# Optimization experiments

Hardware: AMD Instinct MI355X
Metric: run time of the kernel (lower is better)

The kernel has to match this reference:

```python
import jax, jax.numpy as jnp
import numpy as np

N_NODES = 50000


def _sage_conv(x, src, dst, W_l, b_l, W_r):
    # mean aggregation of source-node features at destination nodes
    msg_sum = jax.ops.segment_sum(x[src], dst, num_segments=N_NODES)  # [N, d_in]
    deg = jax.ops.segment_sum(jnp.ones((src.shape[0],), x.dtype), dst,
                              num_segments=N_NODES)  # [N]
    mean = msg_sum / jnp.maximum(deg, 1.0)[:, None]
    # SAGEConv: lin_l(aggr) + lin_r(x); lin_l has bias, lin_r does not
    return mean @ W_l + b_l + x @ W_r


def setup_inputs() -> dict:
    key = jax.random.key(0)
    ks = jax.random.split(key, 8)
    d_in, d_hid, d_out = 128, 128, 64
    E = 800000
    s = lambda k, shp: jax.random.normal(k, shp, dtype=jnp.float32) * (1.0 / np.sqrt(shp[0]))
    return {
        "x": jax.random.normal(ks[0], (N_NODES, d_in), dtype=jnp.float32),
        "edge_index": jax.random.randint(ks[1], (2, E), 0, N_NODES, dtype=jnp.int64
                                         if jax.config.jax_enable_x64 else jnp.int32),
        "W_l1": s(ks[2], (d_in, d_hid)),
        "b_l1": jnp.zeros((d_hid,), jnp.float32),
        "W_r1": s(ks[3], (d_in, d_hid)),
        "W_l2": s(ks[4], (d_hid, d_out)),
        "b_l2": jnp.zeros((d_out,), jnp.float32),
        "W_r2": s(ks[5], (d_hid, d_out)),
    }


def reference(x, edge_index, W_l1, b_l1, W_r1, W_l2, b_l2, W_r2):
    src, dst = edge_index[0], edge_index[1]
    h = _sage_conv(x, src, dst, W_l1, b_l1, W_r1)
    h = jax.nn.relu(h)  # dropout is identity in eval mode
    h = _sage_conv(h, src, dst, W_l2, b_l2, W_r2)
    return h
```

## Files before the change

### kernel.cpp

```cpp
#include <hip/hip_runtime.h>
#include <hip/hip_bf16.h>

#define N_NODES 50000
#define M_TILES 3125
#define NBUCKET 196
#define CAP 5120
#define CHUNK_A 3125
#define CONV_BLOCKS 6250
#define QSCALE 20.0f
#define QINV   0.05f
#define PSCALE 16.0f
#define PINV   0.0625f

typedef __attribute__((ext_vector_type(8))) __bf16 bf16x8;
typedef __attribute__((ext_vector_type(4))) float f32x4;

#define OFF_OFF   0
#define OFFE_OFF  200192
#define EBUF_OFF  400384
#define GCUR_OFF  2407424
#define INV_OFF   3800576
#define XBF_OFF   4000768
#define AGG_OFF   16800768
#define PAIRS_OFF 29600768
#define PBF_OFF   42400768
#define WP1_OFF   48800768
#define WP2_OFF   48866304

__device__ __forceinline__ unsigned bfbits(float f) {
    unsigned u = __float_as_uint(f);
    return (u + 0x7fffu + ((u >> 16) & 1u)) & 0xffff0000u;
}
__device__ __forceinline__ unsigned short bf16r(float f) {
    return (unsigned short)(bfbits(f) >> 16);
}
__device__ __forceinline__ float blo(unsigned u) { return __uint_as_float(u << 16); }
__device__ __forceinline__ float bhi(unsigned u) { return __uint_as_float(u & 0xffff0000u); }

__device__ __forceinline__ unsigned f2i8s(float f, float scale) {
    int q = __float2int_rn(fminf(fmaxf(f * scale, -127.0f), 127.0f));
    return (unsigned)(q & 0xff);
}
__device__ __forceinline__ int sb(unsigned v, int by) {
    return (int)(signed char)((v >> (8 * by)) & 0xffu);
}

__global__ __launch_bounds__(256) void prepA_kernel(const float4* __restrict__ x4,
                                                    uint2* __restrict__ xbf,
                                                    unsigned* __restrict__ xq8,
                                                    const float* __restrict__ Wl1,
                                                    const float* __restrict__ Wr1,
                                                    const float* __restrict__ Wl2,
                                                    const float* __restrict__ Wr2,
                                                    unsigned short* __restrict__ Wp1,
                                                    unsigned short* __restrict__ Wp2,
                                                    const int* __restrict__ src,
                                                    const int* __restrict__ dst,
                                                    int* __restrict__ gcur,
                                                    unsigned* __restrict__ pairs, int E) {
    __shared__ int bh[256];
    __shared__ int lcur[256];
    __shared__ int gb[256];
    __shared__ int sc[256];
    __shared__ unsigned lbuf[3328];
    int bid = blockIdx.x;
    int t = threadIdx.x;
    if (bid < CONV_BLOCKS) {
        int i = bid * 256 + t;
        float4 v = x4[i];
        uint2 o;
        o.x = (bfbits(v.x) >> 16) | bfbits(v.y);
        o.y = (bfbits(v.z) >> 16) | bfbits(v.w);
        xbf[i] = o;
        xq8[i] = f2i8s(v.x, QSCALE) | (f2i8s(v.y, QSCALE) << 8) |
                 (f2i8s(v.z, QSCALE) << 16) | (f2i8s(v.w, QSCALE) << 24);
        return;
    }
    bid -= CONV_BLOCKS;
    if (bid < 128) {
        int idx = bid * 256 + t;
        int k = idx >> 7, n = idx & 127;
        float v = (k < 128) ? Wl1[k * 128 + n] : Wr1[(k - 128) * 128 + n];
        Wp1[((k >> 5) << 12) + (n << 5) + (((k >> 3) & 3) << 3) + (k & 7)] = bf16r(v);
        return;
    }
    bid -= 128;
    if (bid < 64) {
        int idx = bid * 256 + t;
        int k = idx >> 7, n = idx & 127;
        float v = (n < 64) ? Wl2[k * 64 + n] : Wr2[k * 64 + (n - 64)];
        Wp2[((k >> 5) << 12) + (n << 5) + (((k >> 3) & 3) << 3) + (k & 7)] = bf16r(v);
        return;
    }
    bid -= 64;
    int e0 = bid * CHUNK_A;
    int e1 = min(e0 + CHUNK_A, E);
    bh[t] = 0;
    lcur[t] = 0;
    __syncthreads();
    for (int e = e0 + t; e < e1; e += 256) atomicAdd(&bh[dst[e] >> 8], 1);
    __syncthreads();
    int v = bh[t];
    sc[t] = v;
    __syncthreads();
    for (int d = 1; d < 256; d <<= 1) {
        int u = (t >= d) ? sc[t - d] : 0;
        __syncthreads();
        sc[t] += u;
        __syncthreads();
    }
    int lbase = sc[t] - v;
    if (v > 0) gb[t] = t * CAP + atomicAdd(&gcur[t], v);
    bh[t] = lbase;
    __syncthreads();
    for (int e = e0 + t; e < e1; e += 256) {
        int s = src[e], d = dst[e];
        int b = d >> 8;
        int lpos = bh[b] + atomicAdd(&lcur[b], 1);
        lbuf[lpos] = (unsigned)s | ((unsigned)d << 16);
    }
    __syncthreads();
    int T = e1 - e0;
    for (int k = t; k < T; k += 256) {
        unsigned p = lbuf[k];
        int b = p >> 24;
        pairs[gb[b] + (k - bh[b])] = p;
    }
}

__global__ __launch_bounds__(256) void passB_kernel(const int* __restrict__ gcur,
                                                    const unsigned* __restrict__ pairs,
                                                    int* __restrict__ off,
                                                    int* __restrict__ offE,
                                                    float* __restrict__ invdeg,
                                                    unsigned short* __restrict__ ebuf16) {
    __shared__ int sc[256];
    __shared__ int fh[256];
    __shared__ int lcnt[256];
    __shared__ unsigned short lout[CAP];
    int b = blockIdx.x;
    int t = threadIdx.x;
    int gb = b * CAP;
    int W = gcur[b];
    fh[t] = 0;
    __syncthreads();
    for (int k = t; k < W; k += 256) atomicAdd(&fh[(pairs[gb + k] >> 16) & 255], 1);
    __syncthreads();
    int c = fh[t];
    sc[t] = c;
    __syncthreads();
    for (int d = 1; d < 256; d <<= 1) {
        int u = (t >= d) ? sc[t - d] : 0;
        __syncthreads();
        sc[t] += u;
        __syncthreads();
    }
    int excl = sc[t] - c;
    int dg = b * 256 + t;
    if (dg < N_NODES) {
        off[dg] = gb + excl;
        offE[dg] = gb + excl + c;
        invdeg[dg] = 1.0f / fmaxf((float)c, 1.0f);
    }
    lcnt[t] = excl;
    __syncthreads();
    for (int k = t; k < W; k += 256) {
        unsigned p = pairs[gb + k];
        int dl = (p >> 16) & 255;
        int pos = atomicAdd(&lcnt[dl], 1);
        lout[pos] = (unsigned short)(p & 0xffffu);
    }
    __syncthreads();
    for (int k = t; k < W; k += 256) ebuf16[gb + k] = lout[k];
}

__global__ __launch_bounds__(64) void gather1_kernel(const int* __restrict__ off,
                                                     const int* __restrict__ offE,
                                                     const unsigned short* __restrict__ ebuf,
                                                     const float* __restrict__ invdeg,
                                                     const uint2* __restrict__ xq8,
                                                     uint4* __restrict__ aggbf4) {
    int d = blockIdx.x;
    int j = threadIdx.x;
    int g = j >> 4;
    int f = j & 15;
    int lo = off[d], hi = offE[d];
    int a[8] = {0, 0, 0, 0, 0, 0, 0, 0};
    int i = lo + g;
    for (; i + 12 < hi; i += 16) {
        int s0 = ebuf[i], s1 = ebuf[i + 4], s2 = ebuf[i + 8], s3 = ebuf[i + 12];
        uint2 v0 = xq8[(size_t)s0 * 16 + f];
        uint2 v1 = xq8[(size_t)s1 * 16 + f];
        uint2 v2 = xq8[(size_t)s2 * 16 + f];
        uint2 v3 = xq8[(size_t)s3 * 16 + f];
#pragma unroll
        for (int by = 0; by < 4; ++by) {
            a[by]     += sb(v0.x, by) + sb(v1.x, by) + sb(v2.x, by) + sb(v3.x, by);
            a[4 + by] += sb(v0.y, by) + sb(v1.y, by) + sb(v2.y, by) + sb(v3.y, by);
        }
    }
    for (; i < hi; i += 4) {
        uint2 v = xq8[(size_t)ebuf[i] * 16 + f];
#pragma unroll
        for (int by = 0; by < 4; ++by) {
            a[by]     += sb(v.x, by);
            a[4 + by] += sb(v.y, by);
        }
    }
#pragma unroll
    for (int q = 0; q < 8; ++q) {
        a[q] += __shfl_xor(a[q], 16, 64);
        a[q] += __shfl_xor(a[q], 32, 64);
    }
    if (g == 0) {
        float inv = invdeg[d] * QINV;
        uint4 o;
        o.x = (bfbits(a[0] * inv) >> 16) | bfbits(a[1] * inv);
        o.y = (bfbits(a[2] * inv) >> 16) | bfbits(a[3] * inv);
        o.z = (bfbits(a[4] * inv) >> 16) | bfbits(a[5] * inv);
        o.w = (bfbits(a[6] * inv) >> 16) | bfbits(a[7] * inv);
        aggbf4[(size_t)d * 16 + f] = o;
    }
}

__global__ __launch_bounds__(256) void gemmF_kernel(const unsigned short* __restrict__ aggbf,
                                                    const unsigned short* __restrict__ xbf,
                                                    const unsigned short* __restrict__ Wp1,
                                                    const float* __restrict__ b1,
                                                    const unsigned short* __restrict__ Wp2,
                                                    const float* __restrict__ b2,
                                                    unsigned char* __restrict__ pq8,
                                                    float* __restrict__ out) {
    __shared__ unsigned short hsm[4][2][2048];
    int w = threadIdx.x >> 6;
    int pairIdx = blockIdx.x * 4 + w;
    int tile0 = pairIdx * 2;
    int tile1 = tile0 + 1;
    bool act0 = tile0 < M_TILES;
    bool act1 = tile1 < M_TILES;
    int t0 = act0 ? tile0 : 0;
    int t1 = act1 ? tile1 : 0;
    int lane = threadIdx.x & 63;
    int lo16 = lane & 15;
    int kg = lane >> 4;
    int r0 = kg * 4;

    f32x4 accA[8], accB[8];
#pragma unroll
    for (int n = 0; n < 8; ++n) {
        accA[n] = (f32x4){0.f, 0.f, 0.f, 0.f};
        accB[n] = (f32x4){0.f, 0.f, 0.f, 0.f};
    }
    const unsigned short* rowa0 = aggbf + (size_t)(t0 * 16 + lo16) * 128;
    const unsigned short* rowx0 = xbf + (size_t)(t0 * 16 + lo16) * 128;
    const unsigned short* rowa1 = aggbf + (size_t)(t1 * 16 + lo16) * 128;
    const unsigned short* rowx1 = xbf + (size_t)(t1 * 16 + lo16) * 128;
#pragma unroll
    for (int ks = 0; ks < 8; ++ks) {
        int ao = (ks < 4 ? ks * 32 : (ks - 4) * 32) + kg * 8;
        bf16x8 a0 = *reinterpret_cast<const bf16x8*>((ks < 4 ? rowa0 : rowx0) + ao);
        bf16x8 a1 = *reinterpret_cast<const bf16x8*>((ks < 4 ? rowa1 : rowx1) + ao);
        const unsigned short* wbase = Wp1 + ks * 4096 + lo16 * 32 + kg * 8;
#pragma unroll
        for (int n = 0; n < 8; ++n) {
            bf16x8 b = *reinterpret_cast<const bf16x8*>(wbase + n * 512);
            accA[n] = __builtin_amdgcn_mfma_f32_16x16x32_bf16(a0, b, accA[n], 0, 0, 0);
            accB[n] = __builtin_amdgcn_mfma_f32_16x16x32_bf16(a1, b, accB[n], 0, 0, 0);
        }
    }

    unsigned short* hs0 = hsm[w][0];
    unsigned short* hs1 = hsm[w][1];
#pragma unroll
    for (int n = 0; n < 8; ++n) {
        int col = n * 16 + lo16;
        float bv = b1[col];
#pragma unroll
        for (int r = 0; r < 4; ++r) {
            int row = r0 + r;
            int sw = (col ^ ((row & 7) << 3));
            hs0[row * 128 + sw] = bf16r(fmaxf(accA[n][r] + bv, 0.0f));
            hs1[row * 128 + sw] = bf16r(fmaxf(accB[n][r] + bv, 0.0f));
        }
    }
    __syncthreads();

    f32x4 acc2A[8], acc2B[8];
#pragma unroll
    for (int n = 0; n < 8; ++n) {
        acc2A[n] = (f32x4){0.f, 0.f, 0.f, 0.f};
        acc2B[n] = (f32x4){0.f, 0.f, 0.f, 0.f};
    }
#pragma unroll
    for (int ks = 0; ks < 4; ++ks) {
        int base0 = (ks * 32 + kg * 8) ^ ((lo16 & 7) << 3);
        bf16x8 a20 = *reinterpret_cast<const bf16x8*>(&hs0[lo16 * 128 + base0]);
        bf16x8 a21 = *reinterpret_cast<const bf16x8*>(&hs1[lo16 * 128 + base0]);
        const unsigned short* wbase = Wp2 + ks * 4096 + lo16 * 32 + kg * 8;
#pragma unroll
        for (int n = 0; n < 8; ++n) {
            bf16x8 b = *reinterpret_cast<const bf16x8*>(wbase + n * 512);
            acc2A[n] = __builtin_amdgcn_mfma_f32_16x16x32_bf16(a20, b, acc2A[n], 0, 0, 0);
            acc2B[n] = __builtin_amdgcn_mfma_f32_16x16x32_bf16(a21, b, acc2B[n], 0, 0, 0);
        }
    }

#pragma unroll
    for (int n = 0; n < 8; ++n) {
        int col = n * 16 + lo16;
        if (col < 64) {
#pragma unroll
            for (int r = 0; r < 4; ++r) {
                if (act0) pq8[(size_t)(tile0 * 16 + r0 + r) * 64 + col] =
                    (unsigned char)f2i8s(acc2A[n][r], PSCALE);
                if (act1) pq8[(size_t)(tile1 * 16 + r0 + r) * 64 + col] =
                    (unsigned char)f2i8s(acc2B[n][r], PSCALE);
            }
        } else {
            float bv = b2[col - 64];
#pragma unroll
            for (int r = 0; r < 4; ++r) {
                if (act0) out[(size_t)(tile0 * 16 + r0 + r) * 64 + (col - 64)] = acc2A[n][r] + bv;
                if (act1) out[(size_t)(tile1 * 16 + r0 + r) * 64 + (col - 64)] = acc2B[n][r] + bv;
            }
        }
    }
}

__global__ __launch_bounds__(64) void gather2_kernel(const int* __restrict__ off,
                                                     const int* __restrict__ offE,
                                                     const unsigned short* __restrict__ ebuf,
                                                     const float* __restrict__ invdeg,
                                                     const unsigned* __restrict__ pq8,
                                                     float4* __restrict__ out4) {
    int d = blockIdx.x;
    int j = threadIdx.x;
    int g = j >> 4;
    int f = j & 15;
    int lo = off[d], hi = offE[d];
    int a0 = 0, a1 = 0, a2 = 0, a3 = 0;
    int i = lo + g;
    for (; i + 12 < hi; i += 16) {
        int s0 = ebuf[i], s1 = ebuf[i + 4], s2 = ebuf[i + 8], s3 = ebuf[i + 12];
        unsigned v0 = pq8[(size_t)s0 * 16 + f];
        unsigned v1 = pq8[(size_t)s1 * 16 + f];
        unsigned v2 = pq8[(size_t)s2 * 16 + f];
        unsigned v3 = pq8[(size_t)s3 * 16 + f];
        a0 += sb(v0, 0) + sb(v1, 0) + sb(v2, 0) + sb(v3, 0);
        a1 += sb(v0, 1) + sb(v1, 1) + sb(v2, 1) + sb(v3, 1);
        a2 += sb(v0, 2) + sb(v1, 2) + sb(v2, 2) + sb(v3, 2);
        a3 += sb(v0, 3) + sb(v1, 3) + sb(v2, 3) + sb(v3, 3);
    }
    for (; i < hi; i += 4) {
        unsigned v = pq8[(size_t)ebuf[i] * 16 + f];
        a0 += sb(v, 0);
        a1 += sb(v, 1);
        a2 += sb(v, 2);
        a3 += sb(v, 3);
    }
    a0 += __shfl_xor(a0, 16, 64); a0 += __shfl_xor(a0, 32, 64);
    a1 += __shfl_xor(a1, 16, 64); a1 += __shfl_xor(a1, 32, 64);
    a2 += __shfl_xor(a2, 16, 64); a2 += __shfl_xor(a2, 32, 64);
    a3 += __shfl_xor(a3, 16, 64); a3 += __shfl_xor(a3, 32, 64);
    if (g == 0) {
        float inv = invdeg[d] * PINV;
        float4* op = out4 + (size_t)d * 16 + f;
        float4 o = *op;
        o.x += a0 * inv;
        o.y += a1 * inv;
        o.z += a2 * inv;
        o.w += a3 * inv;
        *op = o;
    }
}

extern "C" void kernel_launch(void* const* d_in, const int* in_sizes, int n_in,
                              void* d_out, int out_size, void* d_ws, size_t ws_size,
                              hipStream_t stream) {
    const float* x   = (const float*)d_in[0];
    const int*   ei  = (const int*)d_in[1];
    const float* Wl1 = (const float*)d_in[2];
    const float* b1  = (const float*)d_in[3];
    const float* Wr1 = (const float*)d_in[4];
    const float* Wl2 = (const float*)d_in[5];
    const float* b2  = (const float*)d_in[6];
    const float* Wr2 = (const float*)d_in[7];
    float* out = (float*)d_out;

    const int E = in_sizes[1] / 2;
    const int* src = ei;
    const int* dst = ei + E;

    char* ws = (char*)d_ws;
    int*            off    = (int*)(ws + OFF_OFF);
    int*            offE   = (int*)(ws + OFFE_OFF);
    unsigned short* ebuf16 = (unsigned short*)(ws + EBUF_OFF);
    int*            gcur   = (int*)(ws + GCUR_OFF);
    float*          invdeg = (float*)(ws + INV_OFF);
    unsigned*       xbf    = (unsigned*)(ws + XBF_OFF);
    unsigned*       aggbf  = (unsigned*)(ws + AGG_OFF);
    unsigned*       pairs  = (unsigned*)(ws + PAIRS_OFF);
    unsigned*       xq8    = (unsigned*)(ws + PBF_OFF);
    unsigned char*  pq8    = (unsigned char*)(ws + PBF_OFF);
    unsigned short* Wp1    = (unsigned short*)(ws + WP1_OFF);
    unsigned short* Wp2    = (unsigned short*)(ws + WP2_OFF);

    (void)hipMemsetAsync(gcur, 0, NBUCKET * sizeof(int), stream);

    prepA_kernel<<<CONV_BLOCKS + 192 + 256, 256, 0, stream>>>(
        (const float4*)x, (uint2*)xbf, xq8, Wl1, Wr1, Wl2, Wr2, Wp1, Wp2,
        src, dst, gcur, pairs, E);

    passB_kernel<<<NBUCKET, 256, 0, stream>>>(gcur, pairs, off, offE, invdeg, ebuf16);

    gather1_kernel<<<N_NODES, 64, 0, stream>>>(off, offE, ebuf16, invdeg,
                                               (const uint2*)xq8, (uint4*)aggbf);

    gemmF_kernel<<<(((M_TILES + 1) / 2) + 3) / 4, 256, 0, stream>>>(
        (const unsigned short*)aggbf, (const unsigned short*)xbf,
        Wp1, b1, Wp2, b2, pq8, out);

    gather2_kernel<<<N_NODES, 64, 0, stream>>>(off, offE, ebuf16, invdeg,
                                               (const unsigned*)pq8, (float4*)out);
}
```

Before: 110.4 us.

## Split layer-1 int8 gather into two feature-plane passes and batch nodes per block

```diff
diff --git a/kernel.cpp b/kernel.cpp
--- a/kernel.cpp
+++ b/kernel.cpp
@@ -24,6 +24,7 @@
 #define AGG_OFF   16800768
 #define PAIRS_OFF 29600768
 #define PBF_OFF   42400768
+#define PLANE1_OFF (PBF_OFF + 3200000)
 #define WP1_OFF   48800768
 #define WP2_OFF   48866304
 
@@ -47,7 +48,8 @@
 
 __global__ __launch_bounds__(256) void prepA_kernel(const float4* __restrict__ x4,
                                                     uint2* __restrict__ xbf,
-                                                    unsigned* __restrict__ xq8,
+                                                    unsigned* __restrict__ xq0,
+                                                    unsigned* __restrict__ xq1,
                                                     const float* __restrict__ Wl1,
                                                     const float* __restrict__ Wr1,
                                                     const float* __restrict__ Wl2,
@@ -72,8 +74,11 @@
         o.x = (bfbits(v.x) >> 16) | bfbits(v.y);
         o.y = (bfbits(v.z) >> 16) | bfbits(v.w);
         xbf[i] = o;
-        xq8[i] = f2i8s(v.x, QSCALE) | (f2i8s(v.y, QSCALE) << 8) |
-                 (f2i8s(v.z, QSCALE) << 16) | (f2i8s(v.w, QSCALE) << 24);
+        unsigned q = f2i8s(v.x, QSCALE) | (f2i8s(v.y, QSCALE) << 8) |
+                     (f2i8s(v.z, QSCALE) << 16) | (f2i8s(v.w, QSCALE) << 24);
+        int node = i >> 5, k = i & 31;
+        unsigned* dstp = (k < 16) ? xq0 : xq1;
+        dstp[node * 16 + (k & 15)] = q;
         return;
     }
     bid -= CONV_BLOCKS;
@@ -137,6 +142,7 @@
     __shared__ int sc[256];
     __shared__ int fh[256];
     __shared__ int lcnt[256];
+    __shared__ unsigned lbuf[CAP];
     __shared__ unsigned short lout[CAP];
     int b = blockIdx.x;
     int t = threadIdx.x;
@@ -144,7 +150,11 @@
     int W = gcur[b];
     fh[t] = 0;
     __syncthreads();
-    for (int k = t; k < W; k += 256) atomicAdd(&fh[(pairs[gb + k] >> 16) & 255], 1);
+    for (int k = t; k < W; k += 256) {
+        unsigned p = pairs[gb + k];
+        lbuf[k] = p;
+        atomicAdd(&fh[(p >> 16) & 255], 1);
+    }
     __syncthreads();
     int c = fh[t];
     sc[t] = c;
@@ -165,7 +175,7 @@
     lcnt[t] = excl;
     __syncthreads();
     for (int k = t; k < W; k += 256) {
-        unsigned p = pairs[gb + k];
+        unsigned p = lbuf[k];
         int dl = (p >> 16) & 255;
         int pos = atomicAdd(&lcnt[dl], 1);
         lout[pos] = (unsigned short)(p & 0xffffu);
@@ -174,52 +184,48 @@
     for (int k = t; k < W; k += 256) ebuf16[gb + k] = lout[k];
 }
 
-__global__ __launch_bounds__(64) void gather1_kernel(const int* __restrict__ off,
-                                                     const int* __restrict__ offE,
-                                                     const unsigned short* __restrict__ ebuf,
-                                                     const float* __restrict__ invdeg,
-                                                     const uint2* __restrict__ xq8,
-                                                     uint4* __restrict__ aggbf4) {
-    int d = blockIdx.x;
-    int j = threadIdx.x;
-    int g = j >> 4;
-    int f = j & 15;
-    int lo = off[d], hi = offE[d];
-    int a[8] = {0, 0, 0, 0, 0, 0, 0, 0};
+__global__ __launch_bounds__(256) void gather1_kernel(const int* __restrict__ off,
+                                                      const int* __restrict__ offE,
+                                                      const unsigned short* __restrict__ ebuf,
+                                                      const float* __restrict__ invdeg,
+                                                      const unsigned* __restrict__ xq,
+                                                      unsigned short* __restrict__ agg,
+                                                      int plane) {
+    int node = blockIdx.x * 4 + (threadIdx.x >> 6);
+    int lane = threadIdx.x & 63;
+    int g = lane >> 4;
+    int f = lane & 15;
+    int lo = off[node], hi = offE[node];
+    int a0 = 0, a1 = 0, a2 = 0, a3 = 0;
     int i = lo + g;
     for (; i + 12 < hi; i += 16) {
         int s0 = ebuf[i], s1 = ebuf[i + 4], s2 = ebuf[i + 8], s3 = ebuf[i + 12];
-        uint2 v0 = xq8[(size_t)s0 * 16 + f];
-        uint2 v1 = xq8[(size_t)s1 * 16 + f];
-        uint2 v2 = xq8[(size_t)s2 * 16 + f];
-        uint2 v3 = xq8[(size_t)s3 * 16 + f];
-#pragma unroll
-        for (int by = 0; by < 4; ++by) {
-            a[by]     += sb(v0.x, by) + sb(v1.x, by) + sb(v2.x, by) + sb(v3.x, by);
-            a[4 + by] += sb(v0.y, by) + sb(v1.y, by) + sb(v2.y, by) + sb(v3.y, by);
-        }
+        unsigned v0 = xq[(size_t)s0 * 16 + f];
+        unsigned v1 = xq[(size_t)s1 * 16 + f];
+        unsigned v2 = xq[(size_t)s2 * 16 + f];
+        unsigned v3 = xq[(size_t)s3 * 16 + f];
+        a0 += sb(v0, 0) + sb(v1, 0) + sb(v2, 0) + sb(v3, 0);
+        a1 += sb(v0, 1) + sb(v1, 1) + sb(v2, 1) + sb(v3, 1);
+        a2 += sb(v0, 2) + sb(v1, 2) + sb(v2, 2) + sb(v3, 2);
+        a3 += sb(v0, 3) + sb(v1, 3) + sb(v2, 3) + sb(v3, 3);
     }
     for (; i < hi; i += 4) {
-        uint2 v = xq8[(size_t)ebuf[i] * 16 + f];
-#pragma unroll
-        for (int by = 0; by < 4; ++by) {
-            a[by]     += sb(v.x, by);
-            a[4 + by] += sb(v.y, by);
-        }
-    }
-#pragma unroll
-    for (int q = 0; q < 8; ++q) {
-        a[q] += __shfl_xor(a[q], 16, 64);
-        a[q] += __shfl_xor(a[q], 32, 64);
-    }
+        unsigned v = xq[(size_t)ebuf[i] * 16 + f];
+        a0 += sb(v, 0);
+        a1 += sb(v, 1);
+        a2 += sb(v, 2);
+        a3 += sb(v, 3);
+    }
+    a0 += __shfl_xor(a0, 16, 64); a0 += __shfl_xor(a0, 32, 64);
+    a1 += __shfl_xor(a1, 16, 64); a1 += __shfl_xor(a1, 32, 64);
+    a2 += __shfl_xor(a2, 16, 64); a2 += __shfl_xor(a2, 32, 64);
+    a3 += __shfl_xor(a3, 16, 64); a3 += __shfl_xor(a3, 32, 64);
     if (g == 0) {
-        float inv = invdeg[d] * QINV;
-        uint4 o;
-        o.x = (bfbits(a[0] * inv) >> 16) | bfbits(a[1] * inv);
-        o.y = (bfbits(a[2] * inv) >> 16) | bfbits(a[3] * inv);
-        o.z = (bfbits(a[4] * inv) >> 16) | bfbits(a[5] * inv);
-        o.w = (bfbits(a[6] * inv) >> 16) | bfbits(a[7] * inv);
-        aggbf4[(size_t)d * 16 + f] = o;
+        float inv = invdeg[node] * QINV;
+        uint2 o;
+        o.x = (bfbits(a0 * inv) >> 16) | bfbits(a1 * inv);
+        o.y = (bfbits(a2 * inv) >> 16) | bfbits(a3 * inv);
+        *reinterpret_cast<uint2*>(agg + (size_t)node * 128 + plane * 64 + f * 4) = o;
     }
 }
 
@@ -327,17 +333,17 @@
     }
 }
 
-__global__ __launch_bounds__(64) void gather2_kernel(const int* __restrict__ off,
-                                                     const int* __restrict__ offE,
-                                                     const unsigned short* __restrict__ ebuf,
-                                                     const float* __restrict__ invdeg,
-                                                     const unsigned* __restrict__ pq8,
-                                                     float4* __restrict__ out4) {
-    int d = blockIdx.x;
-    int j = threadIdx.x;
-    int g = j >> 4;
-    int f = j & 15;
-    int lo = off[d], hi = offE[d];
+__global__ __launch_bounds__(256) void gather2_kernel(const int* __restrict__ off,
+                                                      const int* __restrict__ offE,
+                                                      const unsigned short* __restrict__ ebuf,
+                                                      const float* __restrict__ invdeg,
+                                                      const unsigned* __restrict__ pq8,
+                                                      float4* __restrict__ out4) {
+    int node = blockIdx.x * 4 + (threadIdx.x >> 6);
+    int lane = threadIdx.x & 63;
+    int g = lane >> 4;
+    int f = lane & 15;
+    int lo = off[node], hi = offE[node];
     int a0 = 0, a1 = 0, a2 = 0, a3 = 0;
     int i = lo + g;
     for (; i + 12 < hi; i += 16) {
@@ -363,8 +369,8 @@
     a2 += __shfl_xor(a2, 16, 64); a2 += __shfl_xor(a2, 32, 64);
     a3 += __shfl_xor(a3, 16, 64); a3 += __shfl_xor(a3, 32, 64);
     if (g == 0) {
-        float inv = invdeg[d] * PINV;
-        float4* op = out4 + (size_t)d * 16 + f;
+        float inv = invdeg[node] * PINV;
+        float4* op = out4 + (size_t)node * 16 + f;
         float4 o = *op;
         o.x += a0 * inv;
         o.y += a1 * inv;
@@ -398,9 +404,10 @@
     int*            gcur   = (int*)(ws + GCUR_OFF);
     float*          invdeg = (float*)(ws + INV_OFF);
     unsigned*       xbf    = (unsigned*)(ws + XBF_OFF);
-    unsigned*       aggbf  = (unsigned*)(ws + AGG_OFF);
+    unsigned short* aggbf  = (unsigned short*)(ws + AGG_OFF);
     unsigned*       pairs  = (unsigned*)(ws + PAIRS_OFF);
-    unsigned*       xq8    = (unsigned*)(ws + PBF_OFF);
+    unsigned*       xq0    = (unsigned*)(ws + PBF_OFF);
+    unsigned*       xq1    = (unsigned*)(ws + PLANE1_OFF);
     unsigned char*  pq8    = (unsigned char*)(ws + PBF_OFF);
     unsigned short* Wp1    = (unsigned short*)(ws + WP1_OFF);
     unsigned short* Wp2    = (unsigned short*)(ws + WP2_OFF);
@@ -408,18 +415,17 @@
     (void)hipMemsetAsync(gcur, 0, NBUCKET * sizeof(int), stream);
 
     prepA_kernel<<<CONV_BLOCKS + 192 + 256, 256, 0, stream>>>(
-        (const float4*)x, (uint2*)xbf, xq8, Wl1, Wr1, Wl2, Wr2, Wp1, Wp2,
+        (const float4*)x, (uint2*)xbf, xq0, xq1, Wl1, Wr1, Wl2, Wr2, Wp1, Wp2,
         src, dst, gcur, pairs, E);
 
     passB_kernel<<<NBUCKET, 256, 0, stream>>>(gcur, pairs, off, offE, invdeg, ebuf16);
 
-    gather1_kernel<<<N_NODES, 64, 0, stream>>>(off, offE, ebuf16, invdeg,
-                                               (const uint2*)xq8, (uint4*)aggbf);
+    gather1_kernel<<<N_NODES / 4, 256, 0, stream>>>(off, offE, ebuf16, invdeg, xq0, aggbf, 0);
+    gather1_kernel<<<N_NODES / 4, 256, 0, stream>>>(off, offE, ebuf16, invdeg, xq1, aggbf, 1);
 
     gemmF_kernel<<<(((M_TILES + 1) / 2) + 3) / 4, 256, 0, stream>>>(
-        (const unsigned short*)aggbf, (const unsigned short*)xbf,
-        Wp1, b1, Wp2, b2, pq8, out);
-
-    gather2_kernel<<<N_NODES, 64, 0, stream>>>(off, offE, ebuf16, invdeg,
-                                               (const unsigned*)pq8, (float4*)out);
-}
+        aggbf, (const unsigned short*)xbf, Wp1, b1, Wp2, b2, pq8, out);
+
+    gather2_kernel<<<N_NODES / 4, 256, 0, stream>>>(off, offE, ebuf16, invdeg,
+                                                    (const unsigned*)pq8, (float4*)out);
+}
```

Result: slower. 129.1 us (+16.9%).
